# Kernel tuning notes

Measured on AMD Instinct MI355X. Metric: run time of the kernel, lower is better.

The kernel has to match this reference:

```python
import jax, jax.numpy as jnp
import numpy as np

NUM_HEADS = 16
KEY_SIZE = 64
HEAD_SIZE = 64


def setup_inputs() -> dict:
    key = jax.random.key(0)
    ks = jax.random.split(key, 8)
    B, S, D = 2, 2048, 1024
    s = 1.0 / np.sqrt(D)
    return {
        "q": jax.random.normal(ks[0], (B, S, D), jnp.float32),
        "k": jax.random.normal(ks[1], (B, S, D), jnp.float32),
        "v": jax.random.normal(ks[2], (B, S, D), jnp.float32),
        "v_mask": jax.random.randint(ks[3], (B, S), 0, 2, jnp.int32),
        "Wq": jax.random.normal(ks[4], (D, NUM_HEADS * KEY_SIZE), jnp.float32) * s,
        "Wk": jax.random.normal(ks[5], (D, NUM_HEADS * KEY_SIZE), jnp.float32) * s,
        "Wv": jax.random.normal(ks[6], (D, NUM_HEADS * HEAD_SIZE), jnp.float32) * s,
    }


def reference(q, k, v, v_mask, Wq, Wk, Wv):
    B, Sq, _ = q.shape
    Sk = k.shape[1]
    # projections + split heads: [B, S, H, d]
    qw = (q @ Wq).reshape(B, Sq, NUM_HEADS, KEY_SIZE)
    kw = (k @ Wk).reshape(B, Sk, NUM_HEADS, KEY_SIZE)
    vw = (v @ Wv).reshape(B, Sk, NUM_HEADS, HEAD_SIZE)
    # scores [B, H, Sq, Sk]
    a = jnp.einsum('bqhd,bkhd->bhqk', qw, kw) / np.sqrt(KEY_SIZE).astype(np.float32)
    # additive mask over key axis: x*m - (1-m)*1e12
    m = v_mask.astype(a.dtype)[:, None, None, :]
    a = a * m - (1.0 - m) * 1e12
    a = jax.nn.softmax(a, axis=-1)
    # output [B, Sq, H*head_size]
    o = jnp.einsum('bhqk,bkhd->bqhd', a, vw)
    return o.reshape(B, Sq, NUM_HEADS * HEAD_SIZE)
```

## Files before the change

kernel.cpp:

```cpp
#include <hip/hip_runtime.h>
#include <hip/hip_bf16.h>


#define SEQ 2048
#define DIM 1024
#define NPROJ 1024

typedef __bf16 bf16x8 __attribute__((ext_vector_type(8)));
typedef float floatx4 __attribute__((ext_vector_type(4)));
typedef float floatx16 __attribute__((ext_vector_type(16)));

__device__ inline unsigned short f2bf_bits(float x) {
  __hip_bfloat16 h = __float2bfloat16(x);
  return __builtin_bit_cast(unsigned short, h);
}

__device__ __forceinline__ void gload_lds16(const void* g, void* l) {
  __builtin_amdgcn_global_load_lds((const __attribute__((address_space(1))) void*)g,
                                   (__attribute__((address_space(3))) void*)l, 16, 0, 0);
}

__global__ __launch_bounds__(256) void cvt_x(
    const float* __restrict__ q, const float* __restrict__ k, const float* __restrict__ v,
    unsigned short* __restrict__ xb)
{
  const float* X = blockIdx.z == 0 ? q : (blockIdx.z == 1 ? k : v);
  unsigned short* O = xb + (size_t)blockIdx.z * 4096 * 1024;
  int i0 = blockIdx.x * 256 + threadIdx.x;
  #pragma unroll
  for (int it = 0; it < 4; ++it) {
    int i = i0 + it * 262144;
    float4 f = *reinterpret_cast<const float4*>(&X[(size_t)i * 4]);
    ushort4 o;
    o.x = f2bf_bits(f.x); o.y = f2bf_bits(f.y);
    o.z = f2bf_bits(f.z); o.w = f2bf_bits(f.w);
    *reinterpret_cast<ushort4*>(&O[(size_t)i * 4]) = o;
  }
}

__global__ __launch_bounds__(256) void transpose_w(
    const float* __restrict__ Wq, const float* __restrict__ Wk, const float* __restrict__ Wv,
    unsigned short* __restrict__ WqT, unsigned short* __restrict__ WkT, unsigned short* __restrict__ WvT)
{
  const float* W = blockIdx.z == 0 ? Wq : (blockIdx.z == 1 ? Wk : Wv);
  unsigned short* WT = blockIdx.z == 0 ? WqT : (blockIdx.z == 1 ? WkT : WvT);
  const float sc = (blockIdx.z == 0) ? 0.1803368801f : 1.0f;
  __shared__ float tile[64][65];
  const int k0 = blockIdx.x * 64;
  const int n0 = blockIdx.y * 64;
  const int t = threadIdx.x;
  #pragma unroll
  for (int it = 0; it < 4; ++it) {
    int idx = t + (it << 8);
    int r = idx >> 4, c4 = (idx & 15) << 2;
    float4 v = *reinterpret_cast<const float4*>(&W[(k0 + r) * DIM + n0 + c4]);
    tile[r][c4 + 0] = v.x; tile[r][c4 + 1] = v.y;
    tile[r][c4 + 2] = v.z; tile[r][c4 + 3] = v.w;
  }
  __syncthreads();
  #pragma unroll
  for (int it = 0; it < 4; ++it) {
    int idx = t + (it << 8);
    int r = idx >> 4, c4 = (idx & 15) << 2;
    ushort4 o;
    o.x = f2bf_bits(tile[c4 + 0][r] * sc);
    o.y = f2bf_bits(tile[c4 + 1][r] * sc);
    o.z = f2bf_bits(tile[c4 + 2][r] * sc);
    o.w = f2bf_bits(tile[c4 + 3][r] * sc);
    *reinterpret_cast<ushort4*>(&WT[(n0 + r) * DIM + k0 + c4]) = o;
  }
}

__global__ __launch_bounds__(256, 4) void proj_gemm(
    const unsigned short* __restrict__ xb,
    const unsigned short* __restrict__ WqT, const unsigned short* __restrict__ WkT,
    const unsigned short* __restrict__ WvT,
    unsigned short* __restrict__ qw, unsigned short* __restrict__ kw, unsigned short* __restrict__ vw)
{
  const unsigned short* X = xb + (size_t)blockIdx.z * 4096 * 1024;
  const unsigned short* WT = blockIdx.z == 0 ? WqT : (blockIdx.z == 1 ? WkT : WvT);
  unsigned short* Y = blockIdx.z == 0 ? qw : (blockIdx.z == 1 ? kw : vw);

  __shared__ unsigned short Al[2][128 * 32];
  __shared__ unsigned short Bl[2][128 * 32];

  const int m0 = blockIdx.x * 128, n0 = blockIdx.y * 128;
  const int t = threadIdx.x;
  const int lane = t & 63;
  const int wid = t >> 6;
  const int wm = (wid >> 1) << 6, wn = (wid & 1) << 6;
  const int qd = lane >> 4, ln = lane & 15;

  auto stage = [&](int ks, int bi) {
    const int kb = ks << 6;
    #pragma unroll
    for (int i = 0; i < 2; ++i) {
      int p = t + (i << 8);
      int r = p >> 2, c = p & 3;
      int f = (r + (r >> 2)) & 3;
      gload_lds16((const char*)X + (size_t)(m0 + r) * 2048 + kb + ((c ^ f) << 4),
                  (char*)&Al[bi][0] + p * 16);
      gload_lds16((const char*)WT + (size_t)(n0 + r) * 2048 + kb + ((c ^ f) << 4),
                  (char*)&Bl[bi][0] + p * 16);
    }
  };

  floatx4 acc[4][4] = {};
  stage(0, 0);

  for (int ks = 0; ks < 32; ++ks) {
    __syncthreads();
    if (ks + 1 < 32) stage(ks + 1, (ks + 1) & 1);
    const int bi = ks & 1;
    bf16x8 af[4], bfr[4];
    #pragma unroll
    for (int mb = 0; mb < 4; ++mb) {
      int m = wm + mb * 16 + ln;
      int fm = (m + (m >> 2)) & 3;
      af[mb] = *reinterpret_cast<const bf16x8*>(&Al[bi][m * 32 + ((qd ^ fm) << 3)]);
    }
    #pragma unroll
    for (int nb = 0; nb < 4; ++nb) {
      int n = wn + nb * 16 + ln;
      int fn = (n + (n >> 2)) & 3;
      bfr[nb] = *reinterpret_cast<const bf16x8*>(&Bl[bi][n * 32 + ((qd ^ fn) << 3)]);
    }
    #pragma unroll
    for (int mb = 0; mb < 4; ++mb)
      #pragma unroll
      for (int nb = 0; nb < 4; ++nb)
        acc[mb][nb] = __builtin_amdgcn_mfma_f32_16x16x32_bf16(af[mb], bfr[nb], acc[mb][nb], 0, 0, 0);
  }
  #pragma unroll
  for (int mb = 0; mb < 4; ++mb)
    #pragma unroll
    for (int nb = 0; nb < 4; ++nb)
      #pragma unroll
      for (int i = 0; i < 4; ++i) {
        int m = m0 + wm + mb * 16 + qd * 4 + i;
        int n = n0 + wn + nb * 16 + ln;
        Y[(size_t)m * NPROJ + n] = f2bf_bits(acc[mb][nb][i]);
      }
}

__global__ __launch_bounds__(256) void transpose_v(
    const unsigned short* __restrict__ vw, const int* __restrict__ vmask,
    unsigned short* __restrict__ vt, unsigned short* __restrict__ mb)
{
  if (blockIdx.y == 0 && blockIdx.x < 16) {
    int i = blockIdx.x * 256 + threadIdx.x;
    mb[i] = vmask[i] ? 0x3F80 : 0;
  }
  __shared__ unsigned short tile[64 * 64];
  const int t = threadIdx.x;
  const int s0 = blockIdx.x * 64;
  const int bh = blockIdx.y;
  const int b = bh >> 4, h = bh & 15;
  #pragma unroll
  for (int it = 0; it < 2; ++it) {
    int p = t + (it << 8);
    int s = p >> 3, c = p & 7;
    int cp = (c + (s >> 3) + (s & 7)) & 7;
    int4 d = *reinterpret_cast<const int4*>(&vw[(size_t)(b * SEQ + s0 + s) * NPROJ + h * 64 + c * 8]);
    if (vmask[b * SEQ + s0 + s] == 0) { d.x = 0; d.y = 0; d.z = 0; d.w = 0; }
    *reinterpret_cast<int4*>(&tile[s * 64 + cp * 8]) = d;
  }
  __syncthreads();
  #pragma unroll
  for (int it = 0; it < 2; ++it) {
    int d = (t >> 3) + (it << 5), sc = t & 7;
    struct { alignas(16) unsigned short u[8]; } o;
    #pragma unroll
    for (int j = 0; j < 8; ++j) {
      int s = sc * 8 + j;
      int cp = ((d >> 3) + (s >> 3) + (s & 7)) & 7;
      o.u[j] = tile[s * 64 + cp * 8 + (d & 7)];
    }
    *reinterpret_cast<int4*>(&vt[(size_t)(bh * 64 + d) * SEQ + s0 + sc * 8]) =
        *reinterpret_cast<const int4*>(o.u);
  }
}

__global__ __launch_bounds__(256, 2) void attn_fwd(
    const unsigned short* __restrict__ qw, const unsigned short* __restrict__ kw,
    const unsigned short* __restrict__ vt, const unsigned short* __restrict__ mb,
    float* __restrict__ out)
{
  extern __shared__ char smem[];
  unsigned short* Kl = (unsigned short*)smem;
  unsigned short* Vl = (unsigned short*)(smem + 24576);
  unsigned short* Ml = (unsigned short*)(smem + 49152);

  const int t = threadIdx.x, lane = t & 63, wid = t >> 6;
  const int l5 = lane & 31, hi = lane >> 5;
  const int bh = blockIdx.x;
  const int q0 = blockIdx.y * 128;
  const int b = bh >> 4, h = bh & 15;
  const int base = b * SEQ;
  const int wq = wid * 32;

  auto stage = [&](int kt, int bi) {
    const int k0 = kt << 6;
    #pragma unroll
    for (int i = 0; i < 2; ++i) {
      int rb = wid * 16 + i * 8;
      int r = rb + (lane >> 3);
      int rsrc = (r & ~12) | ((r & 4) << 1) | ((r & 8) >> 1);
      int sw = ((lane & 7) ^ (r & 7)) << 4;
      gload_lds16((const char*)kw + ((size_t)((base + k0 + rsrc) * NPROJ + h * 64) << 1) + sw,
                  (char*)&Kl[bi * 4096] + rb * 128);
      gload_lds16((const char*)vt + ((size_t)((bh * 64 + r) * SEQ + k0) << 1) + sw,
                  (char*)&Vl[bi * 4096] + rb * 128);
    }
    if (lane < 2)
      gload_lds16((const char*)mb + ((size_t)(base + k0 + wid * 16 + lane * 8) << 1),
                  (char*)&Ml[bi * 64 + wid * 16]);
  };

  bf16x8 qf[4];
  {
    const unsigned short* qptr =
        qw + (size_t)(base + q0 + wq + l5) * NPROJ + h * 64 + hi * 8;
    #pragma unroll
    for (int kk = 0; kk < 4; ++kk)
      qf[kk] = *reinterpret_cast<const bf16x8*>(qptr + kk * 16);
  }

  floatx16 oa0 = {}, oa1 = {}, la = {};
  stage(0, 0);
  stage(1, 1);

  int bi = 0;
  for (int kt = 0; kt < SEQ / 64; ++kt) {
    if (kt + 1 < SEQ / 64) asm volatile("s_waitcnt vmcnt(5)" ::: "memory");
    else                   asm volatile("s_waitcnt vmcnt(0)" ::: "memory");
    __builtin_amdgcn_s_barrier();
    __builtin_amdgcn_sched_barrier(0);
    int bs = bi + 2; if (bs >= 3) bs -= 3;
    if (kt + 2 < SEQ / 64) stage(kt + 2, bs);

    floatx16 s0 = {}, s1 = {};
    #pragma unroll
    for (int kk = 0; kk < 4; ++kk) {
      int ph = ((kk * 2 + hi) ^ (l5 & 7)) << 3;
      bf16x8 k0f = *reinterpret_cast<const bf16x8*>(&Kl[bi * 4096 + l5 * 64 + ph]);
      bf16x8 k1f = *reinterpret_cast<const bf16x8*>(&Kl[bi * 4096 + (32 + l5) * 64 + ph]);
      s0 = __builtin_amdgcn_mfma_f32_32x32x16_bf16(k0f, qf[kk], s0, 0, 0, 0);
      s1 = __builtin_amdgcn_mfma_f32_32x32x16_bf16(k1f, qf[kk], s1, 0, 0, 0);
    }

    float pe[32];
    #pragma unroll
    for (int r = 0; r < 16; ++r) {
      pe[r]      = __builtin_amdgcn_exp2f(s0[r]);
      pe[16 + r] = __builtin_amdgcn_exp2f(s1[r]);
    }

    #pragma unroll
    for (int kk = 0; kk < 4; ++kk) {
      struct alignas(16) { unsigned short u[8]; } pk;
      #pragma unroll
      for (int j = 0; j < 8; ++j) pk.u[j] = f2bf_bits(pe[8 * kk + j]);
      bf16x8 pa = __builtin_bit_cast(bf16x8, pk);
      int ph = ((kk * 2 + hi) ^ (l5 & 7)) << 3;
      bf16x8 v0 = *reinterpret_cast<const bf16x8*>(&Vl[bi * 4096 + l5 * 64 + ph]);
      bf16x8 v1 = *reinterpret_cast<const bf16x8*>(&Vl[bi * 4096 + (32 + l5) * 64 + ph]);
      bf16x8 mf = *reinterpret_cast<const bf16x8*>(&Ml[bi * 64 + kk * 16 + hi * 8]);
      oa0 = __builtin_amdgcn_mfma_f32_32x32x16_bf16(pa, v0, oa0, 0, 0, 0);
      oa1 = __builtin_amdgcn_mfma_f32_32x32x16_bf16(pa, v1, oa1, 0, 0, 0);
      la  = __builtin_amdgcn_mfma_f32_32x32x16_bf16(pa, mf, la, 0, 0, 0);
    }
    bi = (bi + 1 == 3) ? 0 : bi + 1;
  }

  #pragma unroll
  for (int r = 0; r < 16; ++r) {
    int row = wq + (r & 3) + ((r >> 2) << 3) + (hi << 2);
    float inv = 1.0f / la[r];
    size_t o = (size_t)(base + q0 + row) * NPROJ + h * 64;
    out[o + l5] = oa0[r] * inv;
    out[o + 32 + l5] = oa1[r] * inv;
  }
}

extern "C" void kernel_launch(void* const* d_in, const int* in_sizes, int n_in,
                              void* d_out, int out_size, void* d_ws, size_t ws_size,
                              hipStream_t stream) {
  const float* q  = (const float*)d_in[0];
  const float* k  = (const float*)d_in[1];
  const float* v  = (const float*)d_in[2];
  const int* vm   = (const int*)d_in[3];
  const float* Wq = (const float*)d_in[4];
  const float* Wk = (const float*)d_in[5];
  const float* Wv = (const float*)d_in[6];
  float* out = (float*)d_out;

  unsigned short* ws = (unsigned short*)d_ws;
  unsigned short* WqT = ws + ((size_t)0 << 20);
  unsigned short* WkT = ws + ((size_t)1 << 20);
  unsigned short* WvT = ws + ((size_t)2 << 20);
  unsigned short* qw  = ws + ((size_t)3 << 20);
  unsigned short* kw  = ws + ((size_t)7 << 20);
  unsigned short* vw  = ws + ((size_t)11 << 20);
  unsigned short* xb  = ws + ((size_t)15 << 20);
  unsigned short* vt  = ws + ((size_t)15 << 20);
  unsigned short* mbv = WqT;

  cvt_x<<<dim3(1024, 1, 3), 256, 0, stream>>>(q, k, v, xb);
  transpose_w<<<dim3(16, 16, 3), 256, 0, stream>>>(Wq, Wk, Wv, WqT, WkT, WvT);
  proj_gemm<<<dim3(32, 8, 3), 256, 0, stream>>>(xb, WqT, WkT, WvT, qw, kw, vw);
  transpose_v<<<dim3(32, 32), 256, 0, stream>>>(vw, vm, vt, mbv);
  attn_fwd<<<dim3(32, 16), 256, 49536, stream>>>(qw, kw, vt, mbv, out);
}
```

Baseline: 102.5 us.

## Software-pipeline QK^T one tile ahead with four-stage LDS ring buffer

Restructures the attention main loop so the QK^T MFMAs for tile kt+1 are issued before the exp/PV work of tile kt. This lets the matrix and transcendental work overlap. The LDS ring grows from three to four buffers so the prefetch two tiles ahead does not overwrite the buffer still being read for QK. In exchange it needs more LDS (about 66KB per block) and extra score registers, which may hurt occupancy at two blocks per CU.

After: 102.6 us. No clear change (+0.0%).

```diff
diff --git a/kernel.cpp b/kernel.cpp
--- a/kernel.cpp
+++ b/kernel.cpp
@@ -188,8 +188,8 @@
 {
   extern __shared__ char smem[];
   unsigned short* Kl = (unsigned short*)smem;
-  unsigned short* Vl = (unsigned short*)(smem + 24576);
-  unsigned short* Ml = (unsigned short*)(smem + 49152);
+  unsigned short* Vl = (unsigned short*)(smem + 32768);
+  unsigned short* Ml = (unsigned short*)(smem + 65536);
 
   const int t = threadIdx.x, lane = t & 63, wid = t >> 6;
   const int l5 = lane & 31, hi = lane >> 5;
@@ -198,6 +198,7 @@
   const int b = bh >> 4, h = bh & 15;
   const int base = b * SEQ;
   const int wq = wid * 32;
+  const int NT = SEQ / 64;
 
   auto stage = [&](int kt, int bi) {
     const int k0 = kt << 6;
@@ -226,36 +227,48 @@
       qf[kk] = *reinterpret_cast<const bf16x8*>(qptr + kk * 16);
   }
 
+  auto qk = [&](int bq, floatx16& d0, floatx16& d1) {
+    #pragma unroll
+    for (int kk = 0; kk < 4; ++kk) {
+      int ph = ((kk * 2 + hi) ^ (l5 & 7)) << 3;
+      bf16x8 k0f = *reinterpret_cast<const bf16x8*>(&Kl[bq * 4096 + l5 * 64 + ph]);
+      bf16x8 k1f = *reinterpret_cast<const bf16x8*>(&Kl[bq * 4096 + (32 + l5) * 64 + ph]);
+      d0 = __builtin_amdgcn_mfma_f32_32x32x16_bf16(k0f, qf[kk], d0, 0, 0, 0);
+      d1 = __builtin_amdgcn_mfma_f32_32x32x16_bf16(k1f, qf[kk], d1, 0, 0, 0);
+    }
+  };
+
   floatx16 oa0 = {}, oa1 = {}, la = {};
+  floatx16 sA0 = {}, sA1 = {}, sB0 = {}, sB1 = {};
+
   stage(0, 0);
   stage(1, 1);
-
-  int bi = 0;
-  for (int kt = 0; kt < SEQ / 64; ++kt) {
-    if (kt + 1 < SEQ / 64) asm volatile("s_waitcnt vmcnt(5)" ::: "memory");
-    else                   asm volatile("s_waitcnt vmcnt(0)" ::: "memory");
+  asm volatile("s_waitcnt vmcnt(5)" ::: "memory");
+  __builtin_amdgcn_s_barrier();
+  __builtin_amdgcn_sched_barrier(0);
+  qk(0, sA0, sA1);
+
+  auto iter = [&](int kt, floatx16& sc0, floatx16& sc1, floatx16& sn0, floatx16& sn1) {
+    if (kt + 2 < NT) {
+      stage(kt + 2, (kt + 2) & 3);
+      asm volatile("s_waitcnt vmcnt(5)" ::: "memory");
+    } else {
+      asm volatile("s_waitcnt vmcnt(0)" ::: "memory");
+    }
     __builtin_amdgcn_s_barrier();
     __builtin_amdgcn_sched_barrier(0);
-    int bs = bi + 2; if (bs >= 3) bs -= 3;
-    if (kt + 2 < SEQ / 64) stage(kt + 2, bs);
-
-    floatx16 s0 = {}, s1 = {};
-    #pragma unroll
-    for (int kk = 0; kk < 4; ++kk) {
-      int ph = ((kk * 2 + hi) ^ (l5 & 7)) << 3;
-      bf16x8 k0f = *reinterpret_cast<const bf16x8*>(&Kl[bi * 4096 + l5 * 64 + ph]);
-      bf16x8 k1f = *reinterpret_cast<const bf16x8*>(&Kl[bi * 4096 + (32 + l5) * 64 + ph]);
-      s0 = __builtin_amdgcn_mfma_f32_32x32x16_bf16(k0f, qf[kk], s0, 0, 0, 0);
-      s1 = __builtin_amdgcn_mfma_f32_32x32x16_bf16(k1f, qf[kk], s1, 0, 0, 0);
-    }
+    const int bq = (kt + 1) & 3;
+    const int bv = kt & 3;
+
+    sn0 = (floatx16){}; sn1 = (floatx16){};
+    if (kt + 1 < NT) qk(bq, sn0, sn1);
 
     float pe[32];
     #pragma unroll
     for (int r = 0; r < 16; ++r) {
-      pe[r]      = __builtin_amdgcn_exp2f(s0[r]);
-      pe[16 + r] = __builtin_amdgcn_exp2f(s1[r]);
-    }
-
+      pe[r]      = __builtin_amdgcn_exp2f(sc0[r]);
+      pe[16 + r] = __builtin_amdgcn_exp2f(sc1[r]);
+    }
     #pragma unroll
     for (int kk = 0; kk < 4; ++kk) {
       struct alignas(16) { unsigned short u[8]; } pk;
@@ -263,14 +276,18 @@
       for (int j = 0; j < 8; ++j) pk.u[j] = f2bf_bits(pe[8 * kk + j]);
       bf16x8 pa = __builtin_bit_cast(bf16x8, pk);
       int ph = ((kk * 2 + hi) ^ (l5 & 7)) << 3;
-      bf16x8 v0 = *reinterpret_cast<const bf16x8*>(&Vl[bi * 4096 + l5 * 64 + ph]);
-      bf16x8 v1 = *reinterpret_cast<const bf16x8*>(&Vl[bi * 4096 + (32 + l5) * 64 + ph]);
-      bf16x8 mf = *reinterpret_cast<const bf16x8*>(&Ml[bi * 64 + kk * 16 + hi * 8]);
+      bf16x8 v0 = *reinterpret_cast<const bf16x8*>(&Vl[bv * 4096 + l5 * 64 + ph]);
+      bf16x8 v1 = *reinterpret_cast<const bf16x8*>(&Vl[bv * 4096 + (32 + l5) * 64 + ph]);
+      bf16x8 mf = *reinterpret_cast<const bf16x8*>(&Ml[bv * 64 + kk * 16 + hi * 8]);
       oa0 = __builtin_amdgcn_mfma_f32_32x32x16_bf16(pa, v0, oa0, 0, 0, 0);
       oa1 = __builtin_amdgcn_mfma_f32_32x32x16_bf16(pa, v1, oa1, 0, 0, 0);
       la  = __builtin_amdgcn_mfma_f32_32x32x16_bf16(pa, mf, la, 0, 0, 0);
     }
-    bi = (bi + 1 == 3) ? 0 : bi + 1;
+  };
+
+  for (int kt = 0; kt < NT; kt += 2) {
+    iter(kt,     sA0, sA1, sB0, sB1);
+    iter(kt + 1, sB0, sB1, sA0, sA1);
   }
 
   #pragma unroll
@@ -310,5 +327,5 @@
   transpose_w<<<dim3(16, 16, 3), 256, 0, stream>>>(Wq, Wk, Wv, WqT, WkT, WvT);
   proj_gemm<<<dim3(32, 8, 3), 256, 0, stream>>>(xb, WqT, WkT, WvT, qw, kw, vw);
   transpose_v<<<dim3(32, 32), 256, 0, stream>>>(vw, vm, vt, mbv);
-  attn_fwd<<<dim3(32, 16), 256, 49536, stream>>>(qw, kw, vt, mbv, out);
-}
+  attn_fwd<<<dim3(32, 16), 256, 66048, stream>>>(qw, kw, vt, mbv, out);
+}
```
